# Kernel tuning notes

Measured on AMD Instinct MI355X. Metric: run time of the kernel, lower is better.

## Reference

```python
import jax, jax.numpy as jnp
import numpy as np

B, C_IN, H, W, PAIR_DIM = 4, 23, 256, 512, 64


def setup_inputs() -> dict:
    key = jax.random.key(0)
    k1, k2, k3 = jax.random.split(key, 3)
    msa = jax.random.normal(k1, (B, C_IN, H, W), dtype=jnp.float32)
    # 1x1 Conv2d weight (out, in) and bias, Kaiming-ish scale
    W_conv = jax.random.normal(k2, (PAIR_DIM, C_IN), dtype=jnp.float32) * (1.0 / np.sqrt(C_IN))
    b_conv = jax.random.normal(k3, (PAIR_DIM,), dtype=jnp.float32) * 0.01
    return {"msa": msa, "W_conv": W_conv, "b_conv": b_conv}


def reference(msa, W_conv, b_conv):
    # 1x1 conv == per-position channel mixing: (B,23,H,W) -> (B,C,H,W)
    emb = jnp.einsum("oi,bihw->bohw", W_conv, msa) + b_conv[None, :, None, None]
    emb = jax.nn.relu(emb)
    # mean over MSA depth H distributes over the outer addition:
    # mean_H(emb[...,i,None] + emb[...,None,j]) == avg[...,i,None] + avg[...,None,j]
    avg = emb.mean(axis=2)  # (B, C, W)
    pairs = avg[:, :, :, None] + avg[:, :, None, :]  # (B, C, W, W)
    return jnp.transpose(pairs, (0, 2, 3, 1))  # (B, W, W, C)
```

## Files before the change

### kernel.cpp

```cpp
#include <hip/hip_runtime.h>

#define B_   4
#define CIN  23
#define H_   256
#define W_   512
#define CO   64
#define HC   16
#define NPART (B_ * W_ * CO)

typedef float f32x4 __attribute__((ext_vector_type(4)));
typedef _Float16 half8 __attribute__((ext_vector_type(8)));
typedef unsigned int u32;
typedef u32 u32x4 __attribute__((ext_vector_type(4)));

__global__ __launch_bounds__(256) void conv_mfma_kernel(
    const float* __restrict__ msa,
    const float* __restrict__ Wc,
    const float* __restrict__ bias,
    float* __restrict__ partial)
{
    const int tid  = threadIdx.x;
    const int lane = tid & 63;
    const int wv   = tid >> 6;
    const int wrow = lane & 15;
    const int kg   = lane >> 4;

    const int wq = blockIdx.x;
    const int hc = blockIdx.y;
    const int b  = blockIdx.z;
    const int w0 = wq * 64;

    half8 afrag[4];
#pragma unroll
    for (int g = 0; g < 4; ++g)
#pragma unroll
        for (int j = 0; j < 8; ++j) {
            const int k = 8 * kg + j;
            afrag[g][j] = (_Float16)((k < CIN) ? Wc[(16 * g + wrow) * CIN + k] : 0.f);
        }
    float br[4][4];
#pragma unroll
    for (int g = 0; g < 4; ++g)
#pragma unroll
        for (int r = 0; r < 4; ++r) br[g][r] = bias[16 * g + 4 * kg + r];

    f32x4 acc[4];
#pragma unroll
    for (int g = 0; g < 4; ++g) acc[g] = (f32x4){0.f, 0.f, 0.f, 0.f};

    __shared__ u32 xs[4][12][64];

    const size_t HW = (size_t)H_ * W_;

    for (int s = 0; s < 4; ++s) {
        {
            const int h = hc * 16 + s * 4 + wv;
            const float* src = msa + ((size_t)b * CIN) * HW + (size_t)h * W_ + w0 + lane;
#pragma unroll
            for (int p = 0; p < 12; ++p) {
                const float lo = src[(size_t)(2 * p) * HW];
                const float hi = (2 * p + 1 < CIN) ? src[(size_t)(2 * p + 1) * HW] : 0.f;
                xs[wv][p][(lane + 4 * p) & 63] =
                    __builtin_bit_cast(u32, __builtin_amdgcn_cvt_pkrtz(lo, hi));
            }
        }
        __syncthreads();
        const int wl = 16 * wv + wrow;
#pragma unroll
        for (int hh = 0; hh < 4; ++hh) {
            u32x4 bw;
#pragma unroll
            for (int q = 0; q < 4; ++q) {
                const int p = 4 * kg + q;
                bw[q] = xs[hh][p][(wl + 4 * p) & 63];
            }
            const half8 bfrag = __builtin_bit_cast(half8, bw);
#pragma unroll
            for (int g = 0; g < 4; ++g) {
                f32x4 c = {0.f, 0.f, 0.f, 0.f};
                c = __builtin_amdgcn_mfma_f32_16x16x32_f16(afrag[g], bfrag, c, 0, 0, 0);
#pragma unroll
                for (int r = 0; r < 4; ++r)
                    acc[g][r] += fmaxf(c[r] + br[g][r], 0.f);
            }
        }
        __syncthreads();
    }

    float* dst = partial + (((size_t)hc * B_ + b) * W_ + w0 + 16 * wv + wrow) * CO + 4 * kg;
#pragma unroll
    for (int g = 0; g < 4; ++g)
        *(f32x4*)(dst + 16 * g) = acc[g];
}

__global__ __launch_bounds__(256) void reduce_avg_kernel(
    const float* __restrict__ partial,
    float* __restrict__ avg)
{
    const int idx = blockIdx.x * 256 + threadIdx.x;
    const f32x4* p4 = (const f32x4*)partial;
    f32x4 s = p4[idx];
#pragma unroll
    for (int k = 1; k < HC; ++k) s += p4[(size_t)k * (NPART / 4) + idx];
    ((f32x4*)avg)[idx] = s * (1.0f / H_);
}

__global__ __launch_bounds__(256) void pairs_kernel(
    const float* __restrict__ avg,
    float* __restrict__ out)
{
    const int b   = blockIdx.y;
    const int wi  = blockIdx.x;
    const int tid = threadIdx.x;
    const int cq  = tid & 15;
    const int wj0 = tid >> 4;

    const f32x4* a4 = (const f32x4*)avg;
    const f32x4 aI = a4[(b * W_ + wi) * 16 + cq];
    f32x4* o4 = (f32x4*)out + ((size_t)(b * W_ + wi)) * W_ * 16;

#pragma unroll 4
    for (int wj = wj0; wj < W_; wj += 16) {
        const f32x4 aJ = a4[(b * W_ + wj) * 16 + cq];
        const f32x4 r = aI + aJ;
        __builtin_nontemporal_store(r, o4 + (size_t)wj * 16 + cq);
    }
}

extern "C" void kernel_launch(void* const* d_in, const int* in_sizes, int n_in,
                              void* d_out, int out_size, void* d_ws, size_t ws_size,
                              hipStream_t stream) {
    const float* msa = (const float*)d_in[0];
    const float* Wc  = (const float*)d_in[1];
    const float* bc  = (const float*)d_in[2];
    float* out = (float*)d_out;
    float* avg = (float*)d_ws;

    float* partial = (float*)d_out;

    conv_mfma_kernel<<<dim3(8, HC, B_), 256, 0, stream>>>(msa, Wc, bc, partial);
    reduce_avg_kernel<<<dim3(NPART / 4 / 256), 256, 0, stream>>>(partial, avg);
    pairs_kernel<<<dim3(W_, B_), 256, 0, stream>>>(avg, out);
}
```

Baseline: 78.90 us.

## Load conv operands directly into MFMA fragments without LDS staging

Drops the shared-memory transpose in the conv kernel. Each lane now gathers its 8 input channels straight from global memory into B fragments, with waves split over W halves and H halves. The grid doubles (16x16xB), and the number of H-chunk partials grows from 16 to 32, so the reduce kernel reads twice as much partial data. The pairs kernel switches from nontemporal stores to plain stores and raises its unroll factor. The direct loads give up the coalesced 64-wide rows and barriers of the old path in exchange for strided 16-wide accesses per channel.

Measured after the change: 82.70 us. 4.8% more time.

```diff
diff --git a/kernel.cpp b/kernel.cpp
--- a/kernel.cpp
+++ b/kernel.cpp
@@ -5,7 +5,7 @@
 #define H_   256
 #define W_   512
 #define CO   64
-#define HC   16
+#define HC   32
 #define NPART (B_ * W_ * CO)
 
 typedef float f32x4 __attribute__((ext_vector_type(4)));
@@ -19,16 +19,18 @@
     const float* __restrict__ bias,
     float* __restrict__ partial)
 {
-    const int tid  = threadIdx.x;
-    const int lane = tid & 63;
-    const int wv   = tid >> 6;
-    const int wrow = lane & 15;
-    const int kg   = lane >> 4;
+    const int tid   = threadIdx.x;
+    const int lane  = tid & 63;
+    const int whalf = (tid >> 6) & 1;
+    const int hhalf = tid >> 7;
+    const int wrow  = lane & 15;
+    const int kg    = lane >> 4;
 
-    const int wq = blockIdx.x;
-    const int hc = blockIdx.y;
-    const int b  = blockIdx.z;
-    const int w0 = wq * 64;
+    const int wt  = blockIdx.x;
+    const int hcb = blockIdx.y;
+    const int b   = blockIdx.z;
+    const int w   = wt * 32 + whalf * 16 + wrow;
+    const int h0  = hcb * 16 + hhalf * 8;
 
     half8 afrag[4];
 #pragma unroll
@@ -48,46 +50,39 @@
 #pragma unroll
     for (int g = 0; g < 4; ++g) acc[g] = (f32x4){0.f, 0.f, 0.f, 0.f};
 
-    __shared__ u32 xs[4][12][64];
-
     const size_t HW = (size_t)H_ * W_;
-
-    for (int s = 0; s < 4; ++s) {
-        {
-            const int h = hc * 16 + s * 4 + wv;
-            const float* src = msa + ((size_t)b * CIN) * HW + (size_t)h * W_ + w0 + lane;
+    const float* base = msa + (size_t)b * CIN * HW + (size_t)h0 * W_ + w;
+    const float* src[8];
 #pragma unroll
-            for (int p = 0; p < 12; ++p) {
-                const float lo = src[(size_t)(2 * p) * HW];
-                const float hi = (2 * p + 1 < CIN) ? src[(size_t)(2 * p + 1) * HW] : 0.f;
-                xs[wv][p][(lane + 4 * p) & 63] =
-                    __builtin_bit_cast(u32, __builtin_amdgcn_cvt_pkrtz(lo, hi));
-            }
-        }
-        __syncthreads();
-        const int wl = 16 * wv + wrow;
-#pragma unroll
-        for (int hh = 0; hh < 4; ++hh) {
-            u32x4 bw;
-#pragma unroll
-            for (int q = 0; q < 4; ++q) {
-                const int p = 4 * kg + q;
-                bw[q] = xs[hh][p][(wl + 4 * p) & 63];
-            }
-            const half8 bfrag = __builtin_bit_cast(half8, bw);
-#pragma unroll
-            for (int g = 0; g < 4; ++g) {
-                f32x4 c = {0.f, 0.f, 0.f, 0.f};
-                c = __builtin_amdgcn_mfma_f32_16x16x32_f16(afrag[g], bfrag, c, 0, 0, 0);
-#pragma unroll
-                for (int r = 0; r < 4; ++r)
-                    acc[g][r] += fmaxf(c[r] + br[g][r], 0.f);
-            }
-        }
-        __syncthreads();
+    for (int j = 0; j < 8; ++j) {
+        int k = 8 * kg + j;
+        if (k >= CIN) k = 0;
+        src[j] = base + (size_t)k * HW;
     }
 
-    float* dst = partial + (((size_t)hc * B_ + b) * W_ + w0 + 16 * wv + wrow) * CO + 4 * kg;
+#pragma unroll
+    for (int h = 0; h < 8; ++h) {
+        float x[8];
+#pragma unroll
+        for (int j = 0; j < 8; ++j) x[j] = src[j][h * W_];
+        u32x4 bw;
+#pragma unroll
+        for (int q = 0; q < 4; ++q)
+            bw[q] = __builtin_bit_cast(u32,
+                        __builtin_amdgcn_cvt_pkrtz(x[2 * q], x[2 * q + 1]));
+        const half8 bfrag = __builtin_bit_cast(half8, bw);
+#pragma unroll
+        for (int g = 0; g < 4; ++g) {
+            f32x4 c = {0.f, 0.f, 0.f, 0.f};
+            c = __builtin_amdgcn_mfma_f32_16x16x32_f16(afrag[g], bfrag, c, 0, 0, 0);
+#pragma unroll
+            for (int r = 0; r < 4; ++r)
+                acc[g][r] += fmaxf(c[r] + br[g][r], 0.f);
+        }
+    }
+
+    const int hc = hcb * 2 + hhalf;
+    float* dst = partial + (((size_t)hc * B_ + b) * W_ + w) * CO + 4 * kg;
 #pragma unroll
     for (int g = 0; g < 4; ++g)
         *(f32x4*)(dst + 16 * g) = acc[g];
@@ -119,11 +114,10 @@
     const f32x4 aI = a4[(b * W_ + wi) * 16 + cq];
     f32x4* o4 = (f32x4*)out + ((size_t)(b * W_ + wi)) * W_ * 16;
 
-#pragma unroll 4
+#pragma unroll 8
     for (int wj = wj0; wj < W_; wj += 16) {
         const f32x4 aJ = a4[(b * W_ + wj) * 16 + cq];
-        const f32x4 r = aI + aJ;
-        __builtin_nontemporal_store(r, o4 + (size_t)wj * 16 + cq);
+        o4[(size_t)wj * 16 + cq] = aI + aJ;
     }
 }
 
@@ -138,7 +132,7 @@
 
     float* partial = (float*)d_out;
 
-    conv_mfma_kernel<<<dim3(8, HC, B_), 256, 0, stream>>>(msa, Wc, bc, partial);
+    conv_mfma_kernel<<<dim3(16, 16, B_), 256, 0, stream>>>(msa, Wc, bc, partial);
     reduce_avg_kernel<<<dim3(NPART / 4 / 256), 256, 0, stream>>>(partial, avg);
     pairs_kernel<<<dim3(W_, B_), 256, 0, stream>>>(avg, out);
 }
```
